# Optimization experiments

Measured on AMD Instinct MI355X. Metric: run time of the kernel, lower is better.

The kernel has to match this reference:

```python
import jax, jax.numpy as jnp
import numpy as np

B, S, D = 2, 2048, 1024
H = 16
HD = D // H  # 64
SCALE = HD ** -0.5


def setup_inputs() -> dict:
    key = jax.random.key(0)
    k1, k2, k3 = jax.random.split(key, 3)
    x = jax.random.normal(k1, (B, S, D), dtype=jnp.float32)
    w_qkv = jax.random.normal(k2, (D, 3 * D), dtype=jnp.float32) * (D ** -0.5)
    w_out = jax.random.normal(k3, (D, D), dtype=jnp.float32) * (D ** -0.5)
    return {"x": x, "w_qkv": w_qkv, "w_out": w_out}


def reference(x, w_qkv, w_out):
    batch, seq, hidden = x.shape
    qkv = jnp.einsum('bsd,de->bse', x, w_qkv)  # (B,S,3D)
    q, k, v = jnp.split(qkv, 3, axis=-1)
    # (B,H,S,HD)
    q = q.reshape(batch, seq, H, HD).transpose(0, 2, 1, 3)
    k = k.reshape(batch, seq, H, HD).transpose(0, 2, 1, 3)
    v = v.reshape(batch, seq, H, HD).transpose(0, 2, 1, 3)
    # full (B,H,S,S) scores, as in the original module
    scores = jnp.einsum('bhqd,bhkd->bhqk', q, k) * SCALE
    causal = jnp.tril(jnp.ones((seq, seq), dtype=bool))
    scores = jnp.where(causal[None, None], scores, -jnp.inf)
    attn = jax.nn.softmax(scores, axis=-1)
    out = jnp.einsum('bhqk,bhkd->bhqd', attn, v)
    out = out.transpose(0, 2, 1, 3).reshape(batch, seq, hidden)
    return jnp.einsum('bsd,de->bse', out, w_out)
```

## Files before the change

### kernel.cpp

```cpp
#include <hip/hip_runtime.h>
#include <hip/hip_bf16.h>
#include <stdint.h>

typedef unsigned short u16;
typedef unsigned int u32;
typedef __attribute__((ext_vector_type(8))) short short8;
typedef __attribute__((ext_vector_type(4))) short short4e;
typedef __attribute__((ext_vector_type(4))) float f32x4;
typedef __attribute__((ext_vector_type(16))) float f32x16;

constexpr int CB = 2, CS = 2048, CD = 1024, CH = 16, CHD = 64;
constexpr float SC2 = 0.125f * 1.44269504088896f;
constexpr float DEFER_THR = 11.0f;

__device__ __forceinline__ u16 f2bf(float f) {
    unsigned u = __float_as_uint(f);
    u += 0x7fffu + ((u >> 16) & 1u);
    return (u16)(u >> 16);
}
__device__ __forceinline__ float bf2f(short s) {
    return __uint_as_float(((u32)(unsigned short)s) << 16);
}

#if __has_builtin(__builtin_amdgcn_exp2f)
#define EXP2F(x) __builtin_amdgcn_exp2f(x)
#else
#define EXP2F(x) exp2f(x)
#endif

__device__ __forceinline__ u32 pkbf(float a, float b) {
    u32 r;
    asm("v_cvt_pk_bf16_f32 %0, %1, %2" : "=v"(r) : "v"(a), "v"(b));
    return r;
}

__global__ __launch_bounds__(256) void cvt_x(const float* __restrict__ X, u16* __restrict__ Y) {
    const int i = (blockIdx.x * 256 + threadIdx.x) * 8;
    const float4 v0 = *(const float4*)(X + i);
    const float4 v1 = *(const float4*)(X + i + 4);
    short8 r;
    r[0] = (short)f2bf(v0.x); r[1] = (short)f2bf(v0.y);
    r[2] = (short)f2bf(v0.z); r[3] = (short)f2bf(v0.w);
    r[4] = (short)f2bf(v1.x); r[5] = (short)f2bf(v1.y);
    r[6] = (short)f2bf(v1.z); r[7] = (short)f2bf(v1.w);
    *(short8*)(Y + i) = r;
}

__global__ __launch_bounds__(256) void txw(const float* __restrict__ W, u16* __restrict__ Bt,
                                           int ldw) {
    __shared__ u16 T[64][80];
    const int t = threadIdx.x;
    const int n0 = blockIdx.x * 64, k0 = blockIdx.y * 64;
    const int r = t >> 4, c4 = (t & 15) * 4;
#pragma unroll
    for (int p = 0; p < 4; ++p) {
        const int kr = r + p * 16;
        const float4 v = *(const float4*)(W + (size_t)(k0 + kr) * ldw + n0 + c4);
        T[c4 + 0][kr] = f2bf(v.x); T[c4 + 1][kr] = f2bf(v.y);
        T[c4 + 2][kr] = f2bf(v.z); T[c4 + 3][kr] = f2bf(v.w);
    }
    __syncthreads();
    const int rr = t >> 2, cc = (t & 3) * 16;
    const short8 a = *(const short8*)((const char*)&T[0][0] + rr * 160 + cc * 2);
    const short8 b = *(const short8*)((const char*)&T[0][0] + rr * 160 + cc * 2 + 16);
    u16* dst = Bt + (size_t)(n0 + rr) * 1024 + k0 + cc;
    *(short8*)dst = a;
    *(short8*)(dst + 8) = b;
}

__global__ __launch_bounds__(256) void gemm_mfma(
    const u16* __restrict__ A, const u16* __restrict__ Bt, int mode,
    u16* __restrict__ Qws, u16* __restrict__ Kws, u16* __restrict__ Vtws,
    float* __restrict__ Cf)
{
    __shared__ u16 SB[2][8704];
    const int tid = threadIdx.x;
    const int w = tid >> 6, lane = tid & 63;
    const int l15 = lane & 15, l4 = lane >> 4;
    const int wr = w >> 1, wc = w & 1;
    const int n0 = blockIdx.x * 128, m0 = blockIdx.y * 128;

    f32x4 acc[4][4];
    const f32x4 zf = {0.f, 0.f, 0.f, 0.f};
#pragma unroll
    for (int i = 0; i < 4; ++i)
#pragma unroll
        for (int j = 0; j < 4; ++j) acc[i][j] = zf;

#define GEMM_STAGE(BUF, K0)                                                     \
    {                                                                           \
        _Pragma("unroll")                                                       \
        for (int it = 0; it < 4; ++it) {                                        \
            const int c = tid + it * 256;                                       \
            const u16* src;                                                     \
            if (c < 512) { const int row = c >> 2, cs = c & 3;                  \
                src = A + (size_t)(m0 + row) * 1024 + (K0) + cs * 8; }          \
            else { const int c2 = c - 512; const int row = c2 >> 2, cs = c2 & 3;\
                src = Bt + (size_t)(n0 + row) * 1024 + (K0) + cs * 8; }         \
            __builtin_amdgcn_global_load_lds(                                   \
                (const __attribute__((address_space(1))) unsigned int*)src,     \
                (__attribute__((address_space(3))) unsigned int*)&SB[BUF][c*8], \
                16, 0, 0);                                                      \
        }                                                                       \
    }

    GEMM_STAGE(0, 0);
    __syncthreads();

    for (int t = 0; t < 32; ++t) {
        const int cur = t & 1;
        if (t < 31) GEMM_STAGE(cur ^ 1, (t + 1) * 32);

        const u16* Al = &SB[cur][0];
        const u16* Bl = &SB[cur][4096];
        short8 a[4], b[4];
#pragma unroll
        for (int i = 0; i < 4; ++i)
            a[i] = *(const short8*)(Al + (wr * 64 + i * 16 + l15) * 32 + l4 * 8);
#pragma unroll
        for (int j = 0; j < 4; ++j)
            b[j] = *(const short8*)(Bl + (wc * 64 + j * 16 + l15) * 32 + l4 * 8);
        __builtin_amdgcn_s_setprio(1);
#pragma unroll
        for (int i = 0; i < 4; ++i)
#pragma unroll
            for (int j = 0; j < 4; ++j)
                acc[i][j] = __builtin_amdgcn_mfma_f32_16x16x32_bf16(a[i], b[j], acc[i][j], 0, 0, 0);
        __builtin_amdgcn_s_setprio(0);
        __syncthreads();
    }

    if (mode == 1) {
#pragma unroll
        for (int i = 0; i < 4; ++i)
#pragma unroll
            for (int j = 0; j < 4; ++j)
#pragma unroll
                for (int r = 0; r < 4; ++r)
                    Cf[(size_t)(m0 + wr * 64 + i * 16 + l4 * 4 + r) * 1024 +
                       n0 + wc * 64 + j * 16 + l15] = acc[i][j][r];
    } else {
        const int which = n0 >> 10;
        const int b = m0 >> 11;
        const int sbase = m0 & 2047;
        if (which == 2) {
            const int h = ((n0 >> 6) & 15) + wc;
            const int sb2 = sbase + wr * 64;
#pragma unroll
            for (int i = 0; i < 4; ++i)
#pragma unroll
                for (int j = 0; j < 4; ++j) {
                    const int hd = j * 16 + l15;
                    const int s4 = sb2 + i * 16 + l4 * 4;
                    short4e p;
                    p[0] = (short)f2bf(acc[i][j][0]); p[1] = (short)f2bf(acc[i][j][1]);
                    p[2] = (short)f2bf(acc[i][j][2]); p[3] = (short)f2bf(acc[i][j][3]);
                    *(short4e*)(Vtws + ((size_t)(b * 16 + h) * 64 + hd) * 2048 + s4) = p;
                }
        } else {
            u16* Cl = &SB[0][0];
            const float qsc = which ? 1.0f : SC2;
#pragma unroll
            for (int i = 0; i < 4; ++i)
#pragma unroll
                for (int j = 0; j < 4; ++j)
#pragma unroll
                    for (int r = 0; r < 4; ++r)
                        Cl[(wr * 64 + i * 16 + l4 * 4 + r) * 136 +
                           wc * 64 + j * 16 + l15] = f2bf(acc[i][j][r] * qsc);
            __syncthreads();
            u16* dst = which ? Kws : Qws;
            const int hb = (n0 >> 6) & 15;
#pragma unroll
            for (int it = 0; it < 8; ++it) {
                const int c = tid + it * 256;
                const int row = c >> 4, sub = c & 15;
                const int half = sub >> 3, off = (sub & 7) * 8;
                const short8 v = *(const short8*)(Cl + row * 136 + half * 64 + off);
                *(short8*)(dst + ((size_t)(b * 16 + hb + half) * 2048 + sbase + row) * 64
                               + off) = v;
            }
        }
    }
#undef GEMM_STAGE
}

__global__ __launch_bounds__(256) void attn_seg(
    const u16* __restrict__ Qg, const u16* __restrict__ Kg,
    const u16* __restrict__ Vtg, u16* __restrict__ Og,
    u16* __restrict__ Opart, float* __restrict__ Oml)
{
    __shared__ u16 KV[2][8192];

    static const int jt_of_u[40] = {0,1,2,3, 4,4, 5,5, 6,6, 7,7,
                                    8,8,8, 9,9,9, 10,10,10, 11,11,11,
                                    12,12,12,12, 13,13,13,13, 14,14,14,14, 15,15,15,15};
    static const int seg_of_u[40] = {0,0,0,0, 0,1, 0,1, 0,1, 0,1,
                                     0,1,2, 0,1,2, 0,1,2, 0,1,2,
                                     0,1,2,3, 0,1,2,3, 0,1,2,3, 0,1,2,3};

    const int tid = threadIdx.x;
    const int w = tid >> 6, lane = tid & 63;
    const int l31 = lane & 31, hi = lane >> 5;
    const int bid = blockIdx.x;
    const int u = 39 - (bid >> 5);
    const int bh = bid & 31;
    const int jt = jt_of_u[u], seg = seg_of_u[u];
    const int t0 = seg * 8;
    const int tmax = 2 * jt + 2;
    const int t1 = (tmax < t0 + 8) ? tmax : (t0 + 8);

    const u16* Qp = Qg + (size_t)bh * CS * CHD;
    const u16* Kp = Kg + (size_t)bh * CS * CHD;
    const u16* Vp = Vtg + (size_t)bh * CHD * CS;
    const int q0w = jt * 128 + w * 32;
    const int qrow = q0w + l31;

    short8 qf[4];
#pragma unroll
    for (int c = 0; c < 4; ++c)
        qf[c] = *(const short8*)(Qp + (size_t)qrow * 64 + c * 16 + hi * 8);

    f32x16 o0, o1;
#pragma unroll
    for (int r = 0; r < 16; ++r) { o0[r] = 0.f; o1[r] = 0.f; }
    float m_run = -1e30f, l_run = 0.f;

    short8 stg[4];
#define ATTN_ISSUE(K0)                                                           \
    {                                                                            \
        _Pragma("unroll")                                                        \
        for (int it = 0; it < 4; ++it) {                                         \
            const int c = tid + it * 256;                                        \
            const int ob = c * 16;                                               \
            const u16* src;                                                      \
            if (ob < 8192) { const int row = ob >> 7, cs = (ob >> 4) & 7;        \
                src = Kp + (size_t)((K0) + row) * 64 + cs * 8; }                 \
            else { const int o2 = ob - 8192; const int row = o2 >> 7,            \
                cs = (o2 >> 4) & 7;                                              \
                src = Vp + (size_t)row * CS + (K0) + cs * 8; }                   \
            stg[it] = *(const short8*)src;                                       \
        }                                                                        \
    }
#define ATTN_WRITE(BUF)                                                          \
    {                                                                            \
        _Pragma("unroll")                                                        \
        for (int it = 0; it < 4; ++it) {                                         \
            const int c = tid + it * 256;                                        \
            const int ob = c * 16;                                               \
            int db;                                                              \
            if (ob < 8192) { const int row = ob >> 7; db = ob ^ ((row & 7) << 4); } \
            else { const int o2 = ob - 8192; const int row = o2 >> 7;            \
                db = 8192 + (o2 ^ ((row & 7) << 4)); }                           \
            *(short8*)((char*)&KV[BUF][0] + db) = stg[it];                       \
        }                                                                        \
    }

    ATTN_ISSUE(t0 * 64);
    ATTN_WRITE(0);
    __syncthreads();

    for (int kt = t0; kt < t1; ++kt) {
        const int k0 = kt * 64;
        const int cur = (kt - t0) & 1;
        if (kt + 1 < t1) ATTN_ISSUE((kt + 1) * 64);

        if (k0 <= q0w + 31) {
            const char* Kl = (const char*)&KV[cur][0];
            const char* Vl = (const char*)&KV[cur][4096];
            const bool edge = (k0 + 63 > q0w);
            const bool do_hi = (k0 + 32 <= q0w + 31);

            f32x16 s0, s1;
#pragma unroll
            for (int r = 0; r < 16; ++r) s0[r] = 0.f;
            __builtin_amdgcn_s_setprio(1);
#pragma unroll
            for (int c = 0; c < 4; ++c) {
                const int row = l31;
                const short8 kf = *(const short8*)(Kl + row * 128 +
                                    ((c * 32 + hi * 16) ^ ((row & 7) << 4)));
                s0 = __builtin_amdgcn_mfma_f32_32x32x16_bf16(kf, qf[c], s0, 0, 0, 0);
            }
            if (do_hi) {
#pragma unroll
                for (int r = 0; r < 16; ++r) s1[r] = 0.f;
#pragma unroll
                for (int c = 0; c < 4; ++c) {
                    const int row = 32 + l31;
                    const short8 kf = *(const short8*)(Kl + row * 128 +
                                        ((c * 32 + hi * 16) ^ ((row & 7) << 4)));
                    s1 = __builtin_amdgcn_mfma_f32_32x32x16_bf16(kf, qf[c], s1, 0, 0, 0);
                }
            }
            __builtin_amdgcn_s_setprio(0);

            float pmax = -1e30f;
#pragma unroll
            for (int r = 0; r < 16; ++r) {
                float a0 = s0[r];
                if (edge) {
                    const int koff = (r & 3) + 8 * (r >> 2) + 4 * hi;
                    if (k0 + koff > qrow) a0 = -1e30f;
                }
                s0[r] = a0;
                pmax = fmaxf(pmax, a0);
            }
            if (do_hi) {
#pragma unroll
                for (int r = 0; r < 16; ++r) {
                    float a1 = s1[r];
                    if (edge) {
                        const int koff = (r & 3) + 8 * (r >> 2) + 4 * hi;
                        if (k0 + 32 + koff > qrow) a1 = -1e30f;
                    }
                    s1[r] = a1;
                    pmax = fmaxf(pmax, a1);
                }
            }
            pmax = fmaxf(pmax, __shfl_xor(pmax, 32));

            if (!__all(pmax - m_run <= DEFER_THR)) {
                const float mn = fmaxf(m_run, pmax);
                const float al = EXP2F(m_run - mn);
                l_run *= al;
                m_run = mn;
#pragma unroll
                for (int r = 0; r < 16; ++r) {
                    const int qq = (r & 3) + 8 * (r >> 2) + 4 * hi;
                    const float av = __shfl(al, qq);
                    o0[r] *= av; o1[r] *= av;
                }
            }

            float lsum = 0.f;
#pragma unroll
            for (int r = 0; r < 16; ++r) {
                const float p0 = EXP2F(s0[r] - m_run);
                s0[r] = p0; lsum += p0;
            }
            if (do_hi) {
#pragma unroll
                for (int r = 0; r < 16; ++r) {
                    const float p1 = EXP2F(s1[r] - m_run);
                    s1[r] = p1; lsum += p1;
                }
            }
            lsum += __shfl_xor(lsum, 32);
            l_run += lsum;

#define PV_STEP(KS, SV)                                                          \
            {                                                                    \
                const int rb = ((KS) & 1) * 8;                                   \
                u32 w0 = pkbf(SV[rb + 0], SV[rb + 1]);                           \
                u32 w1 = pkbf(SV[rb + 2], SV[rb + 3]);                           \
                u32 w2 = pkbf(SV[rb + 4], SV[rb + 5]);                           \
                u32 w3 = pkbf(SV[rb + 6], SV[rb + 7]);                           \
                asm("v_permlane32_swap_b32 %0, %1" : "+v"(w0), "+v"(w2));        \
                asm("v_permlane32_swap_b32 %0, %1" : "+v"(w1), "+v"(w3));        \
                union { u32 uw[4]; short8 v; } pu;                               \
                pu.uw[0] = w0; pu.uw[1] = w1; pu.uw[2] = w2; pu.uw[3] = w3;      \
                const short8 pa = pu.v;                                          \
                const int vr0 = l31, vr1 = 32 + l31;                             \
                const short8 v0 = *(const short8*)(Vl + vr0 * 128 +              \
                                    (((KS) * 32 + hi * 16) ^ ((vr0 & 7) << 4))); \
                const short8 v1 = *(const short8*)(Vl + vr1 * 128 +              \
                                    (((KS) * 32 + hi * 16) ^ ((vr1 & 7) << 4))); \
                __builtin_amdgcn_s_setprio(1);                                   \
                o0 = __builtin_amdgcn_mfma_f32_32x32x16_bf16(pa, v0, o0, 0, 0, 0);\
                o1 = __builtin_amdgcn_mfma_f32_32x32x16_bf16(pa, v1, o1, 0, 0, 0);\
                __builtin_amdgcn_s_setprio(0);                                   \
            }
            PV_STEP(0, s0)
            PV_STEP(1, s0)
            if (do_hi) {
                PV_STEP(2, s1)
                PV_STEP(3, s1)
            }
#undef PV_STEP
        }

        if (kt + 1 < t1) ATTN_WRITE(cur ^ 1);
        __syncthreads();
    }

    if (jt < 4) {
        const float invl = 1.f / l_run;
#pragma unroll
        for (int g = 0; g < 4; ++g)
#pragma unroll
            for (int c = 0; c < 4; ++c) {
                const int qq = 8 * g + 4 * hi + c;
                const float av = __shfl(invl, qq);
                u16* dst = Og + ((size_t)(bh >> 4) * CS + jt * 128 + w * 32 + qq) * CD
                             + (bh & 15) * 64 + l31;
                dst[0]  = f2bf(o0[g * 4 + c] * av);
                dst[32] = f2bf(o1[g * 4 + c] * av);
            }
    } else {
        const int slot = bh * 36 + (u - 4);
        u16* pd = Opart + ((size_t)slot * 128 + w * 32) * 64;
#pragma unroll
        for (int g = 0; g < 4; ++g)
#pragma unroll
            for (int c = 0; c < 4; ++c) {
                const int qq = 8 * g + 4 * hi + c;
                pd[qq * 64 + l31]      = f2bf(o0[g * 4 + c]);
                pd[qq * 64 + 32 + l31] = f2bf(o1[g * 4 + c]);
            }
        if (lane < 32) {
            const size_t mi = ((size_t)slot * 128 + w * 32 + l31) * 2;
            Oml[mi]     = m_run;
            Oml[mi + 1] = l_run;
        }
    }
#undef ATTN_ISSUE
#undef ATTN_WRITE
}

__global__ __launch_bounds__(256) void attn_combine(
    const u16* __restrict__ Opart, const float* __restrict__ Oml,
    u16* __restrict__ Og)
{
    static const int ub[16] = {0,1,2,3,4,6,8,10,12,15,18,21,24,28,32,36};
    const int jt = 4 + blockIdx.x;
    const int bh = blockIdx.y;
    const int tid = threadIdx.x;
    const int r = tid >> 1, half = tid & 1;
    const int segs = (jt + 4) >> 2;
    const int slot0 = bh * 36 + ub[jt] - 4;

    float acc[32];
#pragma unroll
    for (int k = 0; k < 32; ++k) acc[k] = 0.f;
    float M = -1e30f, L = 0.f;

    for (int i = 0; i < segs; ++i) {
        const int slot = slot0 + i;
        const float mi = Oml[((size_t)slot * 128 + r) * 2];
        const float li = Oml[((size_t)slot * 128 + r) * 2 + 1];
        float wi;
        if (mi > M) {
            const float sc = EXP2F(M - mi);
#pragma unroll
            for (int k = 0; k < 32; ++k) acc[k] *= sc;
            L *= sc; M = mi; wi = 1.f;
        } else {
            wi = EXP2F(mi - M);
        }
        const u16* op = Opart + ((size_t)slot * 128 + r) * 64 + half * 32;
#pragma unroll
        for (int v = 0; v < 4; ++v) {
            const short8 x = *(const short8*)(op + v * 8);
#pragma unroll
            for (int e = 0; e < 8; ++e)
                acc[v * 8 + e] += wi * bf2f(x[e]);
        }
        L += wi * li;
    }

    const float inv = 1.f / L;
    const int b = bh >> 4, h = bh & 15;
    const int q = jt * 128 + r;
    u16* dst = Og + ((size_t)(b * CS + q)) * CD + h * 64 + half * 32;
#pragma unroll
    for (int v = 0; v < 4; ++v) {
        short8 y;
#pragma unroll
        for (int e = 0; e < 8; ++e) y[e] = (short)f2bf(acc[v * 8 + e] * inv);
        *(short8*)(dst + v * 8) = y;
    }
}

extern "C" void kernel_launch(void* const* d_in, const int* in_sizes, int n_in,
                              void* d_out, int out_size, void* d_ws, size_t ws_size,
                              hipStream_t stream)
{
    const float* x     = (const float*)d_in[0];
    const float* w_qkv = (const float*)d_in[1];
    const float* w_out = (const float*)d_in[2];
    float* out = (float*)d_out;

    u16* xb    = (u16*)d_ws;
    u16* wqkvT = xb    + (size_t)4096 * 1024;
    u16* woutT = wqkvT + (size_t)3072 * 1024;
    u16* Qws   = woutT + (size_t)1024 * 1024;
    u16* Kws   = Qws   + (size_t)32 * 2048 * 64;
    u16* Vtws  = Kws   + (size_t)32 * 2048 * 64;
    u16* Ob    = Vtws  + (size_t)32 * 2048 * 64;
    u16* Opart = Ob    + (size_t)4096 * 1024;
    float* Oml = (float*)(Opart + (size_t)1152 * 128 * 64);

    cvt_x<<<2048, 256, 0, stream>>>(x, xb);
    txw<<<dim3(48, 16), 256, 0, stream>>>(w_qkv, wqkvT, 3072);
    txw<<<dim3(16, 16), 256, 0, stream>>>(w_out, woutT, 1024);

    gemm_mfma<<<dim3(24, 32), 256, 0, stream>>>(xb, wqkvT, 0, Qws, Kws, Vtws, nullptr);
    attn_seg<<<1280, 256, 0, stream>>>(Qws, Kws, Vtws, Ob, Opart, Oml);
    attn_combine<<<dim3(12, 32), 256, 0, stream>>>(Opart, Oml, Ob);
    gemm_mfma<<<dim3(8, 32), 256, 0, stream>>>(Ob, woutT, 1, nullptr, nullptr, nullptr, out);
}
```

Baseline: 201.7 us.

## Merge prep kernels, use async LDS loads in attention, narrower out-proj tiles

Fuses the x conversion and both weight transposes into one prep launch to cut launch overhead. Replaces register-staged K/V loads in the attention kernel with direct global-to-LDS loads, applying the XOR swizzle on the source address instead. Templates the GEMM on tile width and uses 64-wide N tiles for the output projection, doubling its block count for better CU occupancy. Costs are extra branching in prep and smaller per-block reuse in the output GEMM.

Measured after the change: 197.7 us. -2.0%, faster.

```diff
diff --git a/kernel.cpp b/kernel.cpp
--- a/kernel.cpp
+++ b/kernel.cpp
@@ -34,23 +34,33 @@
     return r;
 }
 
-__global__ __launch_bounds__(256) void cvt_x(const float* __restrict__ X, u16* __restrict__ Y) {
-    const int i = (blockIdx.x * 256 + threadIdx.x) * 8;
-    const float4 v0 = *(const float4*)(X + i);
-    const float4 v1 = *(const float4*)(X + i + 4);
-    short8 r;
-    r[0] = (short)f2bf(v0.x); r[1] = (short)f2bf(v0.y);
-    r[2] = (short)f2bf(v0.z); r[3] = (short)f2bf(v0.w);
-    r[4] = (short)f2bf(v1.x); r[5] = (short)f2bf(v1.y);
-    r[6] = (short)f2bf(v1.z); r[7] = (short)f2bf(v1.w);
-    *(short8*)(Y + i) = r;
-}
-
-__global__ __launch_bounds__(256) void txw(const float* __restrict__ W, u16* __restrict__ Bt,
-                                           int ldw) {
+__global__ __launch_bounds__(256) void prep(
+    const float* __restrict__ X, u16* __restrict__ Y,
+    const float* __restrict__ Wq, u16* __restrict__ WqT,
+    const float* __restrict__ Wo, u16* __restrict__ WoT)
+{
     __shared__ u16 T[64][80];
+    const int bid = blockIdx.x;
     const int t = threadIdx.x;
-    const int n0 = blockIdx.x * 64, k0 = blockIdx.y * 64;
+    if (bid < 2048) {
+        const int i = (bid * 256 + t) * 8;
+        const float4 v0 = *(const float4*)(X + i);
+        const float4 v1 = *(const float4*)(X + i + 4);
+        short8 r;
+        r[0] = (short)f2bf(v0.x); r[1] = (short)f2bf(v0.y);
+        r[2] = (short)f2bf(v0.z); r[3] = (short)f2bf(v0.w);
+        r[4] = (short)f2bf(v1.x); r[5] = (short)f2bf(v1.y);
+        r[6] = (short)f2bf(v1.z); r[7] = (short)f2bf(v1.w);
+        *(short8*)(Y + i) = r;
+        return;
+    }
+    const bool qkv = (bid < 2816);
+    const int idx = qkv ? (bid - 2048) : (bid - 2816);
+    const int nb = qkv ? 48 : 16;
+    const int ldw = qkv ? 3072 : 1024;
+    const float* W = qkv ? Wq : Wo;
+    u16* Bt = qkv ? WqT : WoT;
+    const int n0 = (idx % nb) * 64, k0 = (idx / nb) * 64;
     const int r = t >> 4, c4 = (t & 15) * 4;
 #pragma unroll
     for (int p = 0; p < 4; ++p) {
@@ -68,29 +78,33 @@
     *(short8*)(dst + 8) = b;
 }
 
+template<int BN>
 __global__ __launch_bounds__(256) void gemm_mfma(
     const u16* __restrict__ A, const u16* __restrict__ Bt, int mode,
     u16* __restrict__ Qws, u16* __restrict__ Kws, u16* __restrict__ Vtws,
     float* __restrict__ Cf)
 {
-    __shared__ u16 SB[2][8704];
+    constexpr int NJ = BN / 32;
+    constexpr int NCHUNK = (128 + BN) * 32 / 8;
+    constexpr int LDSE = (BN == 128) ? 8704 : (128 + BN) * 32;
+    __shared__ u16 SB[2][LDSE];
     const int tid = threadIdx.x;
     const int w = tid >> 6, lane = tid & 63;
     const int l15 = lane & 15, l4 = lane >> 4;
     const int wr = w >> 1, wc = w & 1;
-    const int n0 = blockIdx.x * 128, m0 = blockIdx.y * 128;
-
-    f32x4 acc[4][4];
+    const int n0 = blockIdx.x * BN, m0 = blockIdx.y * 128;
+
+    f32x4 acc[4][NJ];
     const f32x4 zf = {0.f, 0.f, 0.f, 0.f};
 #pragma unroll
     for (int i = 0; i < 4; ++i)
 #pragma unroll
-        for (int j = 0; j < 4; ++j) acc[i][j] = zf;
+        for (int j = 0; j < NJ; ++j) acc[i][j] = zf;
 
 #define GEMM_STAGE(BUF, K0)                                                     \
     {                                                                           \
         _Pragma("unroll")                                                       \
-        for (int it = 0; it < 4; ++it) {                                        \
+        for (int it = 0; it < NCHUNK / 256; ++it) {                             \
             const int c = tid + it * 256;                                       \
             const u16* src;                                                     \
             if (c < 512) { const int row = c >> 2, cs = c & 3;                  \
@@ -113,18 +127,18 @@
 
         const u16* Al = &SB[cur][0];
         const u16* Bl = &SB[cur][4096];
-        short8 a[4], b[4];
+        short8 a[4], b[NJ];
 #pragma unroll
         for (int i = 0; i < 4; ++i)
             a[i] = *(const short8*)(Al + (wr * 64 + i * 16 + l15) * 32 + l4 * 8);
 #pragma unroll
-        for (int j = 0; j < 4; ++j)
-            b[j] = *(const short8*)(Bl + (wc * 64 + j * 16 + l15) * 32 + l4 * 8);
+        for (int j = 0; j < NJ; ++j)
+            b[j] = *(const short8*)(Bl + (wc * (BN / 2) + j * 16 + l15) * 32 + l4 * 8);
         __builtin_amdgcn_s_setprio(1);
 #pragma unroll
         for (int i = 0; i < 4; ++i)
 #pragma unroll
-            for (int j = 0; j < 4; ++j)
+            for (int j = 0; j < NJ; ++j)
                 acc[i][j] = __builtin_amdgcn_mfma_f32_16x16x32_bf16(a[i], b[j], acc[i][j], 0, 0, 0);
         __builtin_amdgcn_s_setprio(0);
         __syncthreads();
@@ -134,12 +148,12 @@
 #pragma unroll
         for (int i = 0; i < 4; ++i)
 #pragma unroll
-            for (int j = 0; j < 4; ++j)
+            for (int j = 0; j < NJ; ++j)
 #pragma unroll
                 for (int r = 0; r < 4; ++r)
                     Cf[(size_t)(m0 + wr * 64 + i * 16 + l4 * 4 + r) * 1024 +
-                       n0 + wc * 64 + j * 16 + l15] = acc[i][j][r];
-    } else {
+                       n0 + wc * (BN / 2) + j * 16 + l15] = acc[i][j][r];
+    } else if constexpr (BN == 128) {
         const int which = n0 >> 10;
         const int b = m0 >> 11;
         const int sbase = m0 & 2047;
@@ -226,44 +240,32 @@
     for (int r = 0; r < 16; ++r) { o0[r] = 0.f; o1[r] = 0.f; }
     float m_run = -1e30f, l_run = 0.f;
 
-    short8 stg[4];
-#define ATTN_ISSUE(K0)                                                           \
+#define ATTN_GSTAGE(BUF, K0)                                                     \
     {                                                                            \
         _Pragma("unroll")                                                        \
         for (int it = 0; it < 4; ++it) {                                         \
             const int c = tid + it * 256;                                        \
             const int ob = c * 16;                                               \
             const u16* src;                                                      \
-            if (ob < 8192) { const int row = ob >> 7, cs = (ob >> 4) & 7;        \
-                src = Kp + (size_t)((K0) + row) * 64 + cs * 8; }                 \
+            if (ob < 8192) { const int row = ob >> 7, j = (ob >> 4) & 7;         \
+                src = Kp + (size_t)((K0) + row) * 64 + 8 * (j ^ (row & 7)); }    \
             else { const int o2 = ob - 8192; const int row = o2 >> 7,            \
-                cs = (o2 >> 4) & 7;                                              \
-                src = Vp + (size_t)row * CS + (K0) + cs * 8; }                   \
-            stg[it] = *(const short8*)src;                                       \
+                j = (o2 >> 4) & 7;                                               \
+                src = Vp + (size_t)row * CS + (K0) + 8 * (j ^ (row & 7)); }      \
+            __builtin_amdgcn_global_load_lds(                                    \
+                (const __attribute__((address_space(1))) unsigned int*)src,      \
+                (__attribute__((address_space(3))) unsigned int*)&KV[BUF][c*8],  \
+                16, 0, 0);                                                       \
         }                                                                        \
     }
-#define ATTN_WRITE(BUF)                                                          \
-    {                                                                            \
-        _Pragma("unroll")                                                        \
-        for (int it = 0; it < 4; ++it) {                                         \
-            const int c = tid + it * 256;                                        \
-            const int ob = c * 16;                                               \
-            int db;                                                              \
-            if (ob < 8192) { const int row = ob >> 7; db = ob ^ ((row & 7) << 4); } \
-            else { const int o2 = ob - 8192; const int row = o2 >> 7;            \
-                db = 8192 + (o2 ^ ((row & 7) << 4)); }                           \
-            *(short8*)((char*)&KV[BUF][0] + db) = stg[it];                       \
-        }                                                                        \
-    }
-
-    ATTN_ISSUE(t0 * 64);
-    ATTN_WRITE(0);
+
+    ATTN_GSTAGE(0, t0 * 64);
     __syncthreads();
 
     for (int kt = t0; kt < t1; ++kt) {
         const int k0 = kt * 64;
         const int cur = (kt - t0) & 1;
-        if (kt + 1 < t1) ATTN_ISSUE((kt + 1) * 64);
+        if (kt + 1 < t1) ATTN_GSTAGE(cur ^ 1, (kt + 1) * 64);
 
         if (k0 <= q0w + 31) {
             const char* Kl = (const char*)&KV[cur][0];
@@ -380,7 +382,6 @@
 #undef PV_STEP
         }
 
-        if (kt + 1 < t1) ATTN_WRITE(cur ^ 1);
         __syncthreads();
     }
 
@@ -414,8 +415,7 @@
             Oml[mi + 1] = l_run;
         }
     }
-#undef ATTN_ISSUE
-#undef ATTN_WRITE
+#undef ATTN_GSTAGE
 }
 
 __global__ __launch_bounds__(256) void attn_combine(
@@ -460,9 +460,8 @@
     }
 
     const float inv = 1.f / L;
-    const int b = bh >> 4, h = bh & 15;
     const int q = jt * 128 + r;
-    u16* dst = Og + ((size_t)(b * CS + q)) * CD + h * 64 + half * 32;
+    u16* dst = Og + ((size_t)((bh >> 4) * CS + q)) * CD + (bh & 15) * 64 + half * 32;
 #pragma unroll
     for (int v = 0; v < 4; ++v) {
         short8 y;
@@ -491,12 +490,9 @@
     u16* Opart = Ob    + (size_t)4096 * 1024;
     float* Oml = (float*)(Opart + (size_t)1152 * 128 * 64);
 
-    cvt_x<<<2048, 256, 0, stream>>>(x, xb);
-    txw<<<dim3(48, 16), 256, 0, stream>>>(w_qkv, wqkvT, 3072);
-    txw<<<dim3(16, 16), 256, 0, stream>>>(w_out, woutT, 1024);
-
-    gemm_mfma<<<dim3(24, 32), 256, 0, stream>>>(xb, wqkvT, 0, Qws, Kws, Vtws, nullptr);
+    prep<<<3072, 256, 0, stream>>>(x, xb, w_qkv, wqkvT, w_out, woutT);
+    gemm_mfma<128><<<dim3(24, 32), 256, 0, stream>>>(xb, wqkvT, 0, Qws, Kws, Vtws, nullptr);
     attn_seg<<<1280, 256, 0, stream>>>(Qws, Kws, Vtws, Ob, Opart, Oml);
     attn_combine<<<dim3(12, 32), 256, 0, stream>>>(Opart, Oml, Ob);
-    gemm_mfma<<<dim3(8, 32), 256, 0, stream>>>(Ob, woutT, 1, nullptr, nullptr, nullptr, out);
-}
+    gemm_mfma<64><<<dim3(16, 32), 256, 0, stream>>>(Ob, woutT, 1, nullptr, nullptr, nullptr, out);
+}
```
